# Kernel optimization log

Hardware: AMD Instinct MI355X
Metric: run time of the kernel (lower is better)

## Reference

```python
import jax, jax.numpy as jnp
import numpy as np


def swiglu(g, u):
    return jax.nn.silu(g) * u


def setup_inputs() -> dict:
    key = jax.random.key(0)
    ks = jax.random.split(key, 10)
    D, H, E, HS = 2048, 512, 32, 1024
    B, S = 1, 2048
    s = 0.02
    return {
        "x": jax.random.normal(ks[0], (B, S, D), jnp.float32),
        "gate_w": jax.random.normal(ks[1], (E, D), jnp.float32) * s,
        "expert_bias": jnp.zeros((E,), jnp.float32),
        "wg": jax.random.normal(ks[2], (E, D, H), jnp.float32) * s,
        "wu": jax.random.normal(ks[3], (E, D, H), jnp.float32) * s,
        "wd": jax.random.normal(ks[4], (E, H, D), jnp.float32) * s,
        "sg": jax.random.normal(ks[5], (D, HS), jnp.float32) * s,
        "su": jax.random.normal(ks[6], (D, HS), jnp.float32) * s,
        "sd": jax.random.normal(ks[7], (HS, D), jnp.float32) * s,
        "coef_w": jax.random.normal(ks[8], (2, D), jnp.float32) * s,
        "coef_b": jnp.zeros((2,), jnp.float32),
        "top_k": 4,
    }


def reference(x, gate_w, expert_bias, wg, wu, wd, sg, su, sd, coef_w, coef_b, top_k):
    # --- sigmoid router with bias-adjusted top-k selection ---
    logits = jnp.einsum("bsd,ed->bse", x, gate_w)            # [B,S,E]
    routing = jax.nn.sigmoid(logits.astype(jnp.float32))
    biased = routing + expert_bias[None, None, :]
    _, inds = jax.lax.top_k(biased, top_k)                    # [B,S,k]
    scores = jnp.take_along_axis(routing, inds, axis=-1)      # gather UNbiased weights
    scores = scores / (jnp.sum(scores, axis=-1, keepdims=True) + 1e-20)  # norm_topk_prob
    scores = scores.astype(x.dtype)

    # --- SwitchGLU experts: dense per-expert SwiGLU, then gather top-k outputs ---
    h = jnp.einsum("bsd,edh->bseh", x, wg)                    # [B,S,E,H]
    u = jnp.einsum("bsd,edh->bseh", x, wu)
    y_all = jnp.einsum("bseh,ehd->bsed", swiglu(h, u), wd)    # [B,S,E,D]
    expert_out = jnp.take_along_axis(
        y_all, inds[..., None], axis=2)                        # [B,S,k,D]
    y_experts = jnp.sum(expert_out * scores[..., None], axis=-2)  # [B,S,D]

    # --- shared expert + learned 2-way mixing coefficient ---
    shared = swiglu(x @ sg, x @ su) @ sd                      # [B,S,D]
    coef = jax.nn.softmax(jnp.einsum("bsd,cd->bsc", x, coef_w) + coef_b, axis=-1)
    return y_experts * coef[..., :1] + shared * coef[..., 1:]
```

## Files before the change

kernel.cpp:

```cpp
#include <hip/hip_runtime.h>
#include <hip/hip_bf16.h>
#include <stdint.h>

#define S_TOK   2048
#define DMODEL  2048
#define HEXP    512
#define NEXP    32
#define HSH     1024
#define NPAIR   (S_TOK * 4)
#define NT128   96
#define NT64    160

#define M128_NT  0
#define M128_TE  1
#define M128_TP0 (1 + NT128)
#define M128_TM  (1 + 2 * NT128)
#define M64_NT   (1 + 3 * NT128)
#define M64_TE   (M64_NT + 1)
#define M64_TP0  (M64_NT + 1 + NT64)
#define M64_TM   (M64_NT + 1 + 2 * NT64)
#define META_SIZE (M64_NT + 1 + 3 * NT64)

typedef short  s16x8 __attribute__((ext_vector_type(8)));
typedef __bf16 b16x8 __attribute__((ext_vector_type(8)));
typedef float  f32x4 __attribute__((ext_vector_type(4)));

__device__ __forceinline__ f32x4 mfma16x16x32(s16x8 a, s16x8 b, f32x4 c) {
    return __builtin_amdgcn_mfma_f32_16x16x32_bf16(
        __builtin_bit_cast(b16x8, a), __builtin_bit_cast(b16x8, b), c, 0, 0, 0);
}

__device__ __forceinline__ unsigned short f2bf(float f) {
    union { float f; unsigned int u; } v; v.f = f;
    unsigned int u = v.u;
    return (unsigned short)((u + 0x7FFFu + ((u >> 16) & 1u)) >> 16);
}

__device__ __forceinline__ float bf2f(unsigned short b) {
    union { unsigned int u; float f; } v; v.u = ((unsigned int)b) << 16;
    return v.f;
}

__device__ __forceinline__ void gload16(const unsigned short* g, unsigned short* l) {
    __builtin_amdgcn_global_load_lds(
        (const __attribute__((address_space(1))) void*)(uintptr_t)g,
        (__attribute__((address_space(3))) void*)(uintptr_t)l, 16, 0, 0);
}

__device__ __forceinline__ int src_col8(int lane) {
    return 8 * ((lane & 3) ^ ((lane >> 3) & 3));
}
__device__ __forceinline__ int frag_ko(int fr, int fq) {
    return 8 * (fq ^ ((fr >> 1) & 3));
}

__device__ __forceinline__ void tconv_tile(const float* __restrict__ s,
                                           unsigned short* __restrict__ d,
                                           const int K, const int N,
                                           const int k0, const int n0,
                                           unsigned short* pool)
{
    auto T = (unsigned short (*)[84])pool;
    const int tid = threadIdx.x;
    const int n4 = (tid & 15) * 4;
    const int kr = tid >> 4;
#pragma unroll
    for (int i = 0; i < 4; ++i) {
        const int k = kr + i * 16;
        const float4 v = *reinterpret_cast<const float4*>(s + (size_t)(k0 + k) * N + n0 + n4);
        T[n4 + 0][k] = f2bf(v.x);
        T[n4 + 1][k] = f2bf(v.y);
        T[n4 + 2][k] = f2bf(v.z);
        T[n4 + 3][k] = f2bf(v.w);
    }
    __syncthreads();
    const int nw = tid >> 2;
    const int kc = (tid & 3) * 16;
    unsigned short* o = d + (size_t)(n0 + nw) * K + k0 + kc;
#pragma unroll
    for (int j = 0; j < 4; ++j)
        *reinterpret_cast<uint2*>(o + j * 4) =
            *reinterpret_cast<const uint2*>(&T[nw][kc + j * 4]);
}

__global__ __launch_bounds__(256)
void router_kernel(const float* __restrict__ x, const float* __restrict__ gate_w,
                   const float* __restrict__ expert_bias,
                   const float* __restrict__ coef_w, const float* __restrict__ coef_b,
                   int* __restrict__ inds, float* __restrict__ scores,
                   float* __restrict__ coefo)
{
    const int t = blockIdx.x;
    const int tid = threadIdx.x;
    const int lane = tid & 63;
    const int wave = tid >> 6;
    const float* xr = x + (size_t)t * DMODEL;

    float xv[32];
#pragma unroll
    for (int j = 0; j < 32; ++j) xv[j] = xr[lane + 64 * j];

    __shared__ float s_logits[NEXP];
    __shared__ float s_coef[2];

    for (int i = 0; i < 8; ++i) {
        const int e = wave * 8 + i;
        const float* wr = gate_w + (size_t)e * DMODEL;
        float p = 0.f;
#pragma unroll
        for (int j = 0; j < 32; ++j) p += xv[j] * wr[lane + 64 * j];
#pragma unroll
        for (int o = 32; o > 0; o >>= 1) p += __shfl_xor(p, o);
        if (lane == 0) s_logits[e] = p;
    }
    if (wave == 0) {
        for (int c = 0; c < 2; ++c) {
            const float* wr = coef_w + (size_t)c * DMODEL;
            float p = 0.f;
#pragma unroll
            for (int j = 0; j < 32; ++j) p += xv[j] * wr[lane + 64 * j];
#pragma unroll
            for (int o = 32; o > 0; o >>= 1) p += __shfl_xor(p, o);
            if (lane == 0) s_coef[c] = p;
        }
    }
    __syncthreads();
    if (tid == 0) {
        float routing[NEXP], biased[NEXP];
        for (int e = 0; e < NEXP; ++e) {
            const float r = 1.f / (1.f + expf(-s_logits[e]));
            routing[e] = r;
            biased[e] = r + expert_bias[e];
        }
        int sel[4]; float sc[4]; float ssum = 0.f;
        for (int k = 0; k < 4; ++k) {
            int best = 0; float bv = -1e30f;
            for (int e = 0; e < NEXP; ++e)
                if (biased[e] > bv) { bv = biased[e]; best = e; }
            sel[k] = best; sc[k] = routing[best]; ssum += sc[k];
            biased[best] = -1e30f;
        }
        const float inv = 1.f / (ssum + 1e-20f);
        for (int k = 0; k < 4; ++k) {
            inds[t * 4 + k] = sel[k];
            scores[t * 4 + k] = sc[k] * inv;
        }
        const float l0 = s_coef[0] + coef_b[0];
        const float l1 = s_coef[1] + coef_b[1];
        const float m = fmaxf(l0, l1);
        const float e0 = expf(l0 - m), e1 = expf(l1 - m);
        coefo[t * 2 + 0] = e0 / (e0 + e1);
        coefo[t * 2 + 1] = e1 / (e0 + e1);
    }
}

__global__ __launch_bounds__(256)
void xcast_kernel(const float* __restrict__ x, unsigned short* __restrict__ xb)
{
    const int i = (blockIdx.x * 256 + threadIdx.x) * 4;
    const float4 v = *reinterpret_cast<const float4*>(x + i);
    ushort4 o;
    o.x = f2bf(v.x); o.y = f2bf(v.y); o.z = f2bf(v.z); o.w = f2bf(v.w);
    *reinterpret_cast<ushort4*>(xb + i) = o;
}

__global__ __launch_bounds__(256)
void tconv_all_kernel(const float* __restrict__ wg, const float* __restrict__ wu,
                      const float* __restrict__ sg, const float* __restrict__ su,
                      const float* __restrict__ sd,
                      unsigned short* __restrict__ W1, unsigned short* __restrict__ W2,
                      unsigned short* __restrict__ sgb, unsigned short* __restrict__ sub_,
                      unsigned short* __restrict__ sdb)
{
    __shared__ unsigned short pool[64 * 84];
    const int bid = blockIdx.x;
    if (bid < 8192) {
        const int e = bid >> 8, t = bid & 255;
        tconv_tile(wg + (size_t)e * DMODEL * HEXP, W1 + (size_t)e * HEXP * DMODEL,
                   DMODEL, HEXP, ((t >> 3) & 31) * 64, (t & 7) * 64, pool);
    } else if (bid < 16384) {
        const int e = (bid - 8192) >> 8, t = bid & 255;
        tconv_tile(wu + (size_t)e * DMODEL * HEXP, W2 + (size_t)e * HEXP * DMODEL,
                   DMODEL, HEXP, ((t >> 3) & 31) * 64, (t & 7) * 64, pool);
    } else if (bid < 16896) {
        const int t = bid - 16384;
        tconv_tile(sg, sgb, DMODEL, HSH, (t >> 4) * 64, (t & 15) * 64, pool);
    } else if (bid < 17408) {
        const int t = bid - 16896;
        tconv_tile(su, sub_, DMODEL, HSH, (t >> 4) * 64, (t & 15) * 64, pool);
    } else {
        const int t = bid - 17408;
        tconv_tile(sd, sdb, HSH, DMODEL, (t >> 5) * 64, (t & 31) * 64, pool);
    }
}

__global__ __launch_bounds__(256)
void tconv_wd_kernel(const float* __restrict__ wd, unsigned short* __restrict__ wdb)
{
    __shared__ unsigned short pool[64 * 84];
    const int e = blockIdx.x >> 8, t = blockIdx.x & 255;
    tconv_tile(wd + (size_t)e * HEXP * DMODEL, wdb + (size_t)e * DMODEL * HEXP,
               HEXP, DMODEL, (t >> 5) * 64, (t & 31) * 64, pool);
}

__global__ __launch_bounds__(1024)
void group_kernel(const int* __restrict__ inds, const float* __restrict__ scores,
                  int* __restrict__ meta, int* __restrict__ pair_token,
                  float* __restrict__ pair_score, int* __restrict__ tok_pos)
{
    __shared__ int cnt[NEXP];
    __shared__ int off_s[NEXP];
    __shared__ int cur[NEXP];
    const int tid = threadIdx.x;
    if (tid < NEXP) cnt[tid] = 0;
    __syncthreads();
    for (int i = tid; i < NPAIR; i += 1024) atomicAdd(&cnt[inds[i]], 1);
    __syncthreads();
    if (tid == 0) {
        int run = 0, nt1 = 0, nt2 = 0;
        for (int e = 0; e < NEXP; ++e) {
            off_s[e] = run;
            const int c = cnt[e];
            for (int m0 = 0; m0 < c; m0 += 128) {
                meta[M128_TE + nt1] = e;
                meta[M128_TP0 + nt1] = run + m0;
                meta[M128_TM + nt1] = (c - m0 < 128) ? (c - m0) : 128;
                ++nt1;
            }
            for (int m0 = 0; m0 < c; m0 += 64) {
                meta[M64_TE + nt2] = e;
                meta[M64_TP0 + nt2] = run + m0;
                meta[M64_TM + nt2] = (c - m0 < 64) ? (c - m0) : 64;
                ++nt2;
            }
            run += c;
        }
        meta[M128_NT] = nt1;
        meta[M64_NT] = nt2;
    }
    __syncthreads();
    if (tid < NEXP) cur[tid] = off_s[tid];
    __syncthreads();
    for (int i = tid; i < NPAIR; i += 1024) {
        const int e = inds[i];
        const int pos = atomicAdd(&cur[e], 1);
        pair_token[pos] = i >> 2;
        pair_score[pos] = scores[i];
        tok_pos[i] = pos;
    }
}

__global__ __launch_bounds__(256, 4)
void gufused_kernel(const unsigned short* __restrict__ xb,
                    const unsigned short* __restrict__ W1,
                    const unsigned short* __restrict__ W2,
                    unsigned short* __restrict__ act,
                    const int* __restrict__ meta, const int* __restrict__ pair_token,
                    const unsigned short* __restrict__ sgb,
                    const unsigned short* __restrict__ sub_,
                    unsigned short* __restrict__ shact)
{
    __shared__ unsigned short pool[16384];
    const int bid = blockIdx.x;
    const int tid = threadIdx.x;
    const int lane = tid & 63;
    const int wave = tid >> 6;
    const int fr = lane & 15, fq = lane >> 4;
    const int ko = frag_ko(fr, fq);
    const int sub = lane >> 2;
    const int col8 = src_col8(lane);
    const f32x4 zero4 = {0.f, 0.f, 0.f, 0.f};

    if (bid < 8 * NT128) {
        constexpr int NT = DMODEL / 32;
        constexpr int NB = HEXP;
        auto Al  = (unsigned short (*)[128][32])(pool);
        auto Bgl = (unsigned short (*)[64][32])(pool + 8192);
        auto Bul = (unsigned short (*)[64][32])(pool + 12288);

        const int tt = bid >> 3;
        if (tt >= meta[M128_NT]) return;
        const int e = meta[M128_TE + tt];
        const int p0 = meta[M128_TP0 + tt];
        const int mval = meta[M128_TM + tt];
        const size_t eoff = (size_t)e * NB * DMODEL;
        const unsigned short* Bg = W1 + eoff;
        const unsigned short* Bu = W2 + eoff;
        const int n0 = (bid & 7) * 64;

        const int arow0 = wave * 32 + sub;
        int q0 = p0 + arow0; if (q0 > NPAIR - 1) q0 = NPAIR - 1;
        int q1 = p0 + arow0 + 16; if (q1 > NPAIR - 1) q1 = NPAIR - 1;
        const unsigned short* asrc0 = xb + (size_t)pair_token[q0] * DMODEL + col8;
        const unsigned short* asrc1 = xb + (size_t)pair_token[q1] * DMODEL + col8;
        const int brow = wave * 16 + sub;
        const unsigned short* gsrc = Bg + (size_t)(n0 + brow) * DMODEL + col8;
        const unsigned short* usrc = Bu + (size_t)(n0 + brow) * DMODEL + col8;

        auto stage = [&](int buf, int k0) {
            gload16(asrc0 + k0, &Al[buf][wave * 32][0]);
            gload16(asrc1 + k0, &Al[buf][wave * 32 + 16][0]);
            gload16(gsrc + k0, &Bgl[buf][wave * 16][0]);
            gload16(usrc + k0, &Bul[buf][wave * 16][0]);
        };

        const int wm = wave >> 1, wn = wave & 1;
        f32x4 hacc[4][2], uacc[4][2];
#pragma unroll
        for (int m = 0; m < 4; ++m)
#pragma unroll
            for (int n = 0; n < 2; ++n) { hacc[m][n] = zero4; uacc[m][n] = zero4; }

        auto compute = [&](int buf) {
            s16x8 af[4], bg[2], bu[2];
#pragma unroll
            for (int m = 0; m < 4; ++m)
                af[m] = *reinterpret_cast<const s16x8*>(&Al[buf][wm * 64 + m * 16 + fr][ko]);
#pragma unroll
            for (int n = 0; n < 2; ++n) {
                bg[n] = *reinterpret_cast<const s16x8*>(&Bgl[buf][wn * 32 + n * 16 + fr][ko]);
                bu[n] = *reinterpret_cast<const s16x8*>(&Bul[buf][wn * 32 + n * 16 + fr][ko]);
            }
#pragma unroll
            for (int m = 0; m < 4; ++m)
#pragma unroll
                for (int n = 0; n < 2; ++n) {
                    hacc[m][n] = mfma16x16x32(af[m], bg[n], hacc[m][n]);
                    uacc[m][n] = mfma16x16x32(af[m], bu[n], uacc[m][n]);
                }
        };

        stage(0, 0);
        __syncthreads();
#pragma unroll 1
        for (int t = 0; t < NT; ++t) {
            const int cur = t & 1;
            if (t + 1 < NT) stage(cur ^ 1, (t + 1) * 32);
            compute(cur);
            __syncthreads();
        }

#pragma unroll
        for (int m = 0; m < 4; ++m)
#pragma unroll
            for (int n = 0; n < 2; ++n) {
                const int col = n0 + wn * 32 + n * 16 + fr;
#pragma unroll
                for (int r = 0; r < 4; ++r) {
                    const int rt = wm * 64 + m * 16 + fq * 4 + r;
                    if (rt < mval) {
                        const float hv = hacc[m][n][r];
                        const float a = hv / (1.f + __expf(-hv)) * uacc[m][n][r];
                        act[(size_t)(p0 + rt) * NB + col] = f2bf(a);
                    }
                }
            }
    } else {
        constexpr int NT = DMODEL / 32;
        constexpr int NB = HSH;
        auto Al  = (unsigned short (*)[64][32])(pool);
        auto Bgl = (unsigned short (*)[64][32])(pool + 4096);
        auto Bul = (unsigned short (*)[64][32])(pool + 8192);

        const int idx = bid - 8 * NT128;
        const int p0 = (idx >> 4) * 64;
        const int n0 = (idx & 15) * 64;

        const int arow = wave * 16 + sub;
        const unsigned short* asrc = xb + (size_t)(p0 + arow) * DMODEL + col8;
        const unsigned short* gsrc = sgb + (size_t)(n0 + arow) * DMODEL + col8;
        const unsigned short* usrc = sub_ + (size_t)(n0 + arow) * DMODEL + col8;

        auto stage = [&](int buf, int k0) {
            gload16(asrc + k0, &Al[buf][wave * 16][0]);
            gload16(gsrc + k0, &Bgl[buf][wave * 16][0]);
            gload16(usrc + k0, &Bul[buf][wave * 16][0]);
        };

        const int wm = wave >> 1, wn = wave & 1;
        f32x4 hacc[2][2], uacc[2][2];
#pragma unroll
        for (int m = 0; m < 2; ++m)
#pragma unroll
            for (int n = 0; n < 2; ++n) { hacc[m][n] = zero4; uacc[m][n] = zero4; }

        auto compute = [&](int buf) {
            s16x8 af[2], bg[2], bu[2];
#pragma unroll
            for (int m = 0; m < 2; ++m)
                af[m] = *reinterpret_cast<const s16x8*>(&Al[buf][wm * 32 + m * 16 + fr][ko]);
#pragma unroll
            for (int n = 0; n < 2; ++n) {
                bg[n] = *reinterpret_cast<const s16x8*>(&Bgl[buf][wn * 32 + n * 16 + fr][ko]);
                bu[n] = *reinterpret_cast<const s16x8*>(&Bul[buf][wn * 32 + n * 16 + fr][ko]);
            }
#pragma unroll
            for (int m = 0; m < 2; ++m)
#pragma unroll
                for (int n = 0; n < 2; ++n) {
                    hacc[m][n] = mfma16x16x32(af[m], bg[n], hacc[m][n]);
                    uacc[m][n] = mfma16x16x32(af[m], bu[n], uacc[m][n]);
                }
        };

        stage(0, 0);
        __syncthreads();
#pragma unroll 1
        for (int t = 0; t < NT; ++t) {
            const int cur = t & 1;
            if (t + 1 < NT) stage(cur ^ 1, (t + 1) * 32);
            compute(cur);
            __syncthreads();
        }

#pragma unroll
        for (int m = 0; m < 2; ++m)
#pragma unroll
            for (int n = 0; n < 2; ++n) {
                const int col = n0 + wn * 32 + n * 16 + fr;
#pragma unroll
                for (int r = 0; r < 4; ++r) {
                    const int rt = wm * 32 + m * 16 + fq * 4 + r;
                    const float hv = hacc[m][n][r];
                    const float a = hv / (1.f + __expf(-hv)) * uacc[m][n][r];
                    shact[(size_t)(p0 + rt) * NB + col] = f2bf(a);
                }
            }
    }
}

__global__ __launch_bounds__(256, 4)
void downfused_kernel(const unsigned short* __restrict__ act,
                      const unsigned short* __restrict__ shact,
                      const unsigned short* __restrict__ wdb,
                      const unsigned short* __restrict__ sdb,
                      unsigned short* __restrict__ ypair,
                      float* __restrict__ sdown,
                      const int* __restrict__ meta,
                      const float* __restrict__ pair_score)
{
    __shared__ unsigned short Al[2][64][32];
    __shared__ unsigned short Bl[2][64][32];
    const int bid = blockIdx.x;
    const int tid = threadIdx.x;
    const int lane = tid & 63;
    const int wave = tid >> 6;
    const int fr = lane & 15, fq = lane >> 4;
    const int ko = frag_ko(fr, fq);
    const int sub = lane >> 2;
    const int col8 = src_col8(lane);
    const int wm = wave >> 1, wn = wave & 1;
    const f32x4 zero4 = {0.f, 0.f, 0.f, 0.f};

    const bool EXPERT = bid < 32 * NT64;
    int p0, mval, n0, KA;
    const unsigned short *Asrc, *Bd;
    if (EXPERT) {
        const int tt = bid >> 5;
        if (tt >= meta[M64_NT]) return;
        const int e = meta[M64_TE + tt];
        p0 = meta[M64_TP0 + tt];
        mval = meta[M64_TM + tt];
        n0 = (bid & 31) * 64;
        KA = HEXP;
        Asrc = act;
        Bd = wdb + (size_t)e * DMODEL * HEXP;
    } else {
        const int idx = bid - 32 * NT64;
        p0 = (idx >> 5) * 64;
        mval = 64;
        n0 = (idx & 31) * 64;
        KA = HSH;
        Asrc = shact;
        Bd = sdb;
    }
    const int NT = KA / 32;

    const int arow = wave * 16 + sub;
    int ar = p0 + arow;
    if (EXPERT && ar > NPAIR - 1) ar = NPAIR - 1;
    const unsigned short* asrc = Asrc + (size_t)ar * KA + col8;
    const unsigned short* bsrc = Bd + (size_t)(n0 + arow) * KA + col8;

    auto stage = [&](int buf, int k0) {
        gload16(asrc + k0, &Al[buf][wave * 16][0]);
        gload16(bsrc + k0, &Bl[buf][wave * 16][0]);
    };

    f32x4 acc[2][2];
#pragma unroll
    for (int m = 0; m < 2; ++m)
#pragma unroll
        for (int n = 0; n < 2; ++n) acc[m][n] = zero4;

    auto compute = [&](int buf) {
        s16x8 af[2], bf[2];
#pragma unroll
        for (int m = 0; m < 2; ++m)
            af[m] = *reinterpret_cast<const s16x8*>(&Al[buf][wm * 32 + m * 16 + fr][ko]);
#pragma unroll
        for (int n = 0; n < 2; ++n)
            bf[n] = *reinterpret_cast<const s16x8*>(&Bl[buf][wn * 32 + n * 16 + fr][ko]);
#pragma unroll
        for (int m = 0; m < 2; ++m)
#pragma unroll
            for (int n = 0; n < 2; ++n)
                acc[m][n] = mfma16x16x32(af[m], bf[n], acc[m][n]);
    };

    stage(0, 0);
    __syncthreads();
#pragma unroll 1
    for (int t = 0; t < NT; ++t) {
        const int cur = t & 1;
        if (t + 1 < NT) stage(cur ^ 1, (t + 1) * 32);
        compute(cur);
        __syncthreads();
    }

#pragma unroll
    for (int m = 0; m < 2; ++m)
#pragma unroll
        for (int n = 0; n < 2; ++n) {
            const int col = n0 + wn * 32 + n * 16 + fr;
#pragma unroll
            for (int r = 0; r < 4; ++r) {
                const int rt = wm * 32 + m * 16 + fq * 4 + r;
                if (rt < mval) {
                    if (EXPERT) {
                        const int p = p0 + rt;
                        ypair[(size_t)p * DMODEL + col] = f2bf(acc[m][n][r] * pair_score[p]);
                    } else {
                        sdown[(size_t)(p0 + rt) * DMODEL + col] = acc[m][n][r];
                    }
                }
            }
        }
}

__global__ __launch_bounds__(256)
void final_kernel(const unsigned short* __restrict__ ypair,
                  const float* __restrict__ sdown,
                  const float* __restrict__ coef, const int* __restrict__ tok_pos,
                  float* __restrict__ out)
{
    const int row = blockIdx.x;
    const int col = threadIdx.x * 8;
    float acc[8] = {0.f, 0.f, 0.f, 0.f, 0.f, 0.f, 0.f, 0.f};
#pragma unroll
    for (int k = 0; k < 4; ++k) {
        const int pos = tok_pos[row * 4 + k];
        const uint4 v = *reinterpret_cast<const uint4*>(ypair + (size_t)pos * DMODEL + col);
        const unsigned short* u = reinterpret_cast<const unsigned short*>(&v);
#pragma unroll
        for (int j = 0; j < 8; ++j) acc[j] += bf2f(u[j]);
    }
    const float c0 = coef[row * 2 + 0];
    const float c1 = coef[row * 2 + 1];
    const float* sd = sdown + (size_t)row * DMODEL + col;
    const float4 s0 = *reinterpret_cast<const float4*>(sd);
    const float4 s1 = *reinterpret_cast<const float4*>(sd + 4);
    float4 o0, o1;
    o0.x = acc[0] * c0 + s0.x * c1; o0.y = acc[1] * c0 + s0.y * c1;
    o0.z = acc[2] * c0 + s0.z * c1; o0.w = acc[3] * c0 + s0.w * c1;
    o1.x = acc[4] * c0 + s1.x * c1; o1.y = acc[5] * c0 + s1.y * c1;
    o1.z = acc[6] * c0 + s1.z * c1; o1.w = acc[7] * c0 + s1.w * c1;
    float* op = out + (size_t)row * DMODEL + col;
    *reinterpret_cast<float4*>(op) = o0;
    *reinterpret_cast<float4*>(op + 4) = o1;
}

extern "C" void kernel_launch(void* const* d_in, const int* in_sizes, int n_in,
                              void* d_out, int out_size, void* d_ws, size_t ws_size,
                              hipStream_t stream)
{
    const float* x           = (const float*)d_in[0];
    const float* gate_w      = (const float*)d_in[1];
    const float* expert_bias = (const float*)d_in[2];
    const float* wg          = (const float*)d_in[3];
    const float* wu          = (const float*)d_in[4];
    const float* wd          = (const float*)d_in[5];
    const float* sg          = (const float*)d_in[6];
    const float* su          = (const float*)d_in[7];
    const float* sd          = (const float*)d_in[8];
    const float* coef_w      = (const float*)d_in[9];
    const float* coef_b      = (const float*)d_in[10];
    float* out = (float*)d_out;

    char* ws = (char*)d_ws;
    size_t off = 0;
    auto take = [&](size_t bytes) {
        char* p = ws + off;
        off = (off + bytes + 255) & ~(size_t)255;
        return p;
    };
    int*   inds     = (int*)  take((size_t)S_TOK * 4 * sizeof(int));
    float* scores   = (float*)take((size_t)S_TOK * 4 * sizeof(float));
    float* coefp    = (float*)take((size_t)S_TOK * 2 * sizeof(float));
    int*   meta     = (int*)  take((size_t)META_SIZE * sizeof(int));
    int*   pair_tok = (int*)  take((size_t)NPAIR * sizeof(int));
    float* pair_sc  = (float*)take((size_t)NPAIR * sizeof(float));
    int*   tok_pos  = (int*)  take((size_t)NPAIR * sizeof(int));
    unsigned short* xb    = (unsigned short*)take((size_t)S_TOK * DMODEL * 2);
    unsigned short* act   = (unsigned short*)take((size_t)NPAIR * HEXP * 2);
    unsigned short* shact = (unsigned short*)take((size_t)S_TOK * HSH * 2);
    unsigned short* ypair = (unsigned short*)take((size_t)NPAIR * DMODEL * 2);
    float*          sdown = (float*)take((size_t)S_TOK * DMODEL * 4);
    unsigned short* sgb   = (unsigned short*)take((size_t)HSH * DMODEL * 2);
    unsigned short* sub_  = (unsigned short*)take((size_t)HSH * DMODEL * 2);
    unsigned short* sdb   = (unsigned short*)take((size_t)DMODEL * HSH * 2);
    unsigned short* W1    = (unsigned short*)take((size_t)NEXP * DMODEL * HEXP * 2);
    unsigned short* W2    = (unsigned short*)take((size_t)NEXP * DMODEL * HEXP * 2);
    (void)ws_size; (void)in_sizes; (void)n_in; (void)out_size;

    router_kernel<<<S_TOK, 256, 0, stream>>>(x, gate_w, expert_bias, coef_w, coef_b,
                                             inds, scores, coefp);
    xcast_kernel<<<(S_TOK * DMODEL / 4) / 256, 256, 0, stream>>>(x, xb);
    group_kernel<<<1, 1024, 0, stream>>>(inds, scores, meta, pair_tok, pair_sc, tok_pos);

    tconv_all_kernel<<<17920, 256, 0, stream>>>(wg, wu, sg, su, sd,
                                                W1, W2, sgb, sub_, sdb);

    gufused_kernel<<<8 * NT128 + 512, 256, 0, stream>>>(
        xb, W1, W2, act, meta, pair_tok, sgb, sub_, shact);

    tconv_wd_kernel<<<NEXP * 256, 256, 0, stream>>>(wd, W1);

    downfused_kernel<<<32 * NT64 + 1024, 256, 0, stream>>>(
        act, shact, W1, sdb, ypair, sdown, meta, pair_sc);

    final_kernel<<<S_TOK, 256, 0, stream>>>(ypair, sdown, coefp, tok_pos, out);
}
```

Baseline: 360.5 us.

## Use 128x128 GEMM tiles for gate/up and down, split SwiGLU into separate pass

Gate and up projections now run as separate 128x128-tile GEMMs that write bf16 h and u to scratch buffers. A new elementwise kernel applies SwiGLU to produce the activations. The down projection moves from 64x64 to 128x128 tiles on the 128-row expert grouping, and the 64-row metadata is removed. Larger tiles raise arithmetic intensity and reuse of each loaded tile, at the cost of an extra round trip through memory for h/u, an extra kernel launch, more padding waste on partial expert tiles, and higher register pressure (launch bounds reduced to 3).

```diff
diff --git a/kernel.cpp b/kernel.cpp
--- a/kernel.cpp
+++ b/kernel.cpp
@@ -9,17 +9,12 @@
 #define HSH     1024
 #define NPAIR   (S_TOK * 4)
 #define NT128   96
-#define NT64    160
 
 #define M128_NT  0
 #define M128_TE  1
 #define M128_TP0 (1 + NT128)
 #define M128_TM  (1 + 2 * NT128)
-#define M64_NT   (1 + 3 * NT128)
-#define M64_TE   (M64_NT + 1)
-#define M64_TP0  (M64_NT + 1 + NT64)
-#define M64_TM   (M64_NT + 1 + 2 * NT64)
-#define META_SIZE (M64_NT + 1 + 3 * NT64)
+#define META_SIZE (1 + 3 * NT128)
 
 typedef short  s16x8 __attribute__((ext_vector_type(8)));
 typedef __bf16 b16x8 __attribute__((ext_vector_type(8)));
@@ -217,7 +212,7 @@
     for (int i = tid; i < NPAIR; i += 1024) atomicAdd(&cnt[inds[i]], 1);
     __syncthreads();
     if (tid == 0) {
-        int run = 0, nt1 = 0, nt2 = 0;
+        int run = 0, nt1 = 0;
         for (int e = 0; e < NEXP; ++e) {
             off_s[e] = run;
             const int c = cnt[e];
@@ -227,16 +222,9 @@
                 meta[M128_TM + nt1] = (c - m0 < 128) ? (c - m0) : 128;
                 ++nt1;
             }
-            for (int m0 = 0; m0 < c; m0 += 64) {
-                meta[M64_TE + nt2] = e;
-                meta[M64_TP0 + nt2] = run + m0;
-                meta[M64_TM + nt2] = (c - m0 < 64) ? (c - m0) : 64;
-                ++nt2;
-            }
             run += c;
         }
         meta[M128_NT] = nt1;
-        meta[M64_NT] = nt2;
     }
     __syncthreads();
     if (tid < NEXP) cur[tid] = off_s[tid];
@@ -250,197 +238,20 @@
     }
 }
 
-__global__ __launch_bounds__(256, 4)
-void gufused_kernel(const unsigned short* __restrict__ xb,
-                    const unsigned short* __restrict__ W1,
-                    const unsigned short* __restrict__ W2,
-                    unsigned short* __restrict__ act,
-                    const int* __restrict__ meta, const int* __restrict__ pair_token,
-                    const unsigned short* __restrict__ sgb,
-                    const unsigned short* __restrict__ sub_,
-                    unsigned short* __restrict__ shact)
-{
-    __shared__ unsigned short pool[16384];
-    const int bid = blockIdx.x;
-    const int tid = threadIdx.x;
-    const int lane = tid & 63;
-    const int wave = tid >> 6;
-    const int fr = lane & 15, fq = lane >> 4;
-    const int ko = frag_ko(fr, fq);
-    const int sub = lane >> 2;
-    const int col8 = src_col8(lane);
-    const f32x4 zero4 = {0.f, 0.f, 0.f, 0.f};
-
-    if (bid < 8 * NT128) {
-        constexpr int NT = DMODEL / 32;
-        constexpr int NB = HEXP;
-        auto Al  = (unsigned short (*)[128][32])(pool);
-        auto Bgl = (unsigned short (*)[64][32])(pool + 8192);
-        auto Bul = (unsigned short (*)[64][32])(pool + 12288);
-
-        const int tt = bid >> 3;
-        if (tt >= meta[M128_NT]) return;
-        const int e = meta[M128_TE + tt];
-        const int p0 = meta[M128_TP0 + tt];
-        const int mval = meta[M128_TM + tt];
-        const size_t eoff = (size_t)e * NB * DMODEL;
-        const unsigned short* Bg = W1 + eoff;
-        const unsigned short* Bu = W2 + eoff;
-        const int n0 = (bid & 7) * 64;
-
-        const int arow0 = wave * 32 + sub;
-        int q0 = p0 + arow0; if (q0 > NPAIR - 1) q0 = NPAIR - 1;
-        int q1 = p0 + arow0 + 16; if (q1 > NPAIR - 1) q1 = NPAIR - 1;
-        const unsigned short* asrc0 = xb + (size_t)pair_token[q0] * DMODEL + col8;
-        const unsigned short* asrc1 = xb + (size_t)pair_token[q1] * DMODEL + col8;
-        const int brow = wave * 16 + sub;
-        const unsigned short* gsrc = Bg + (size_t)(n0 + brow) * DMODEL + col8;
-        const unsigned short* usrc = Bu + (size_t)(n0 + brow) * DMODEL + col8;
-
-        auto stage = [&](int buf, int k0) {
-            gload16(asrc0 + k0, &Al[buf][wave * 32][0]);
-            gload16(asrc1 + k0, &Al[buf][wave * 32 + 16][0]);
-            gload16(gsrc + k0, &Bgl[buf][wave * 16][0]);
-            gload16(usrc + k0, &Bul[buf][wave * 16][0]);
-        };
-
-        const int wm = wave >> 1, wn = wave & 1;
-        f32x4 hacc[4][2], uacc[4][2];
-#pragma unroll
-        for (int m = 0; m < 4; ++m)
-#pragma unroll
-            for (int n = 0; n < 2; ++n) { hacc[m][n] = zero4; uacc[m][n] = zero4; }
-
-        auto compute = [&](int buf) {
-            s16x8 af[4], bg[2], bu[2];
-#pragma unroll
-            for (int m = 0; m < 4; ++m)
-                af[m] = *reinterpret_cast<const s16x8*>(&Al[buf][wm * 64 + m * 16 + fr][ko]);
-#pragma unroll
-            for (int n = 0; n < 2; ++n) {
-                bg[n] = *reinterpret_cast<const s16x8*>(&Bgl[buf][wn * 32 + n * 16 + fr][ko]);
-                bu[n] = *reinterpret_cast<const s16x8*>(&Bul[buf][wn * 32 + n * 16 + fr][ko]);
-            }
-#pragma unroll
-            for (int m = 0; m < 4; ++m)
-#pragma unroll
-                for (int n = 0; n < 2; ++n) {
-                    hacc[m][n] = mfma16x16x32(af[m], bg[n], hacc[m][n]);
-                    uacc[m][n] = mfma16x16x32(af[m], bu[n], uacc[m][n]);
-                }
-        };
-
-        stage(0, 0);
-        __syncthreads();
-#pragma unroll 1
-        for (int t = 0; t < NT; ++t) {
-            const int cur = t & 1;
-            if (t + 1 < NT) stage(cur ^ 1, (t + 1) * 32);
-            compute(cur);
-            __syncthreads();
-        }
-
-#pragma unroll
-        for (int m = 0; m < 4; ++m)
-#pragma unroll
-            for (int n = 0; n < 2; ++n) {
-                const int col = n0 + wn * 32 + n * 16 + fr;
-#pragma unroll
-                for (int r = 0; r < 4; ++r) {
-                    const int rt = wm * 64 + m * 16 + fq * 4 + r;
-                    if (rt < mval) {
-                        const float hv = hacc[m][n][r];
-                        const float a = hv / (1.f + __expf(-hv)) * uacc[m][n][r];
-                        act[(size_t)(p0 + rt) * NB + col] = f2bf(a);
-                    }
-                }
-            }
-    } else {
-        constexpr int NT = DMODEL / 32;
-        constexpr int NB = HSH;
-        auto Al  = (unsigned short (*)[64][32])(pool);
-        auto Bgl = (unsigned short (*)[64][32])(pool + 4096);
-        auto Bul = (unsigned short (*)[64][32])(pool + 8192);
-
-        const int idx = bid - 8 * NT128;
-        const int p0 = (idx >> 4) * 64;
-        const int n0 = (idx & 15) * 64;
-
-        const int arow = wave * 16 + sub;
-        const unsigned short* asrc = xb + (size_t)(p0 + arow) * DMODEL + col8;
-        const unsigned short* gsrc = sgb + (size_t)(n0 + arow) * DMODEL + col8;
-        const unsigned short* usrc = sub_ + (size_t)(n0 + arow) * DMODEL + col8;
-
-        auto stage = [&](int buf, int k0) {
-            gload16(asrc + k0, &Al[buf][wave * 16][0]);
-            gload16(gsrc + k0, &Bgl[buf][wave * 16][0]);
-            gload16(usrc + k0, &Bul[buf][wave * 16][0]);
-        };
-
-        const int wm = wave >> 1, wn = wave & 1;
-        f32x4 hacc[2][2], uacc[2][2];
-#pragma unroll
-        for (int m = 0; m < 2; ++m)
-#pragma unroll
-            for (int n = 0; n < 2; ++n) { hacc[m][n] = zero4; uacc[m][n] = zero4; }
-
-        auto compute = [&](int buf) {
-            s16x8 af[2], bg[2], bu[2];
-#pragma unroll
-            for (int m = 0; m < 2; ++m)
-                af[m] = *reinterpret_cast<const s16x8*>(&Al[buf][wm * 32 + m * 16 + fr][ko]);
-#pragma unroll
-            for (int n = 0; n < 2; ++n) {
-                bg[n] = *reinterpret_cast<const s16x8*>(&Bgl[buf][wn * 32 + n * 16 + fr][ko]);
-                bu[n] = *reinterpret_cast<const s16x8*>(&Bul[buf][wn * 32 + n * 16 + fr][ko]);
-            }
-#pragma unroll
-            for (int m = 0; m < 2; ++m)
-#pragma unroll
-                for (int n = 0; n < 2; ++n) {
-                    hacc[m][n] = mfma16x16x32(af[m], bg[n], hacc[m][n]);
-                    uacc[m][n] = mfma16x16x32(af[m], bu[n], uacc[m][n]);
-                }
-        };
-
-        stage(0, 0);
-        __syncthreads();
-#pragma unroll 1
-        for (int t = 0; t < NT; ++t) {
-            const int cur = t & 1;
-            if (t + 1 < NT) stage(cur ^ 1, (t + 1) * 32);
-            compute(cur);
-            __syncthreads();
-        }
-
-#pragma unroll
-        for (int m = 0; m < 2; ++m)
-#pragma unroll
-            for (int n = 0; n < 2; ++n) {
-                const int col = n0 + wn * 32 + n * 16 + fr;
-#pragma unroll
-                for (int r = 0; r < 4; ++r) {
-                    const int rt = wm * 32 + m * 16 + fq * 4 + r;
-                    const float hv = hacc[m][n][r];
-                    const float a = hv / (1.f + __expf(-hv)) * uacc[m][n][r];
-                    shact[(size_t)(p0 + rt) * NB + col] = f2bf(a);
-                }
-            }
-    }
-}
-
-__global__ __launch_bounds__(256, 4)
-void downfused_kernel(const unsigned short* __restrict__ act,
-                      const unsigned short* __restrict__ shact,
-                      const unsigned short* __restrict__ wdb,
-                      const unsigned short* __restrict__ sdb,
-                      unsigned short* __restrict__ ypair,
-                      float* __restrict__ sdown,
-                      const int* __restrict__ meta,
-                      const float* __restrict__ pair_score)
-{
-    __shared__ unsigned short Al[2][64][32];
-    __shared__ unsigned short Bl[2][64][32];
+__global__ __launch_bounds__(256, 3)
+void gu128_kernel(const unsigned short* __restrict__ xb,
+                  const unsigned short* __restrict__ W1,
+                  const unsigned short* __restrict__ W2,
+                  const int* __restrict__ meta, const int* __restrict__ pair_token,
+                  const unsigned short* __restrict__ sgb,
+                  const unsigned short* __restrict__ sub_,
+                  unsigned short* __restrict__ hexp, unsigned short* __restrict__ uexp,
+                  unsigned short* __restrict__ shh, unsigned short* __restrict__ shu)
+{
+    constexpr int NT = DMODEL / 32;
+    __shared__ unsigned short Al[2][128][32];
+    __shared__ unsigned short Bl[2][128][32];
+
     const int bid = blockIdx.x;
     const int tid = threadIdx.x;
     const int lane = tid & 63;
@@ -452,59 +263,71 @@
     const int wm = wave >> 1, wn = wave & 1;
     const f32x4 zero4 = {0.f, 0.f, 0.f, 0.f};
 
-    const bool EXPERT = bid < 32 * NT64;
-    int p0, mval, n0, KA;
-    const unsigned short *Asrc, *Bd;
+    const bool EXPERT = bid < 8 * NT128;
+    int p0, mval, n0, NB;
+    const unsigned short* B;
+    unsigned short* obuf;
+    int tok0, tok1;
+    const int arow0 = wave * 32 + sub;
     if (EXPERT) {
-        const int tt = bid >> 5;
-        if (tt >= meta[M64_NT]) return;
-        const int e = meta[M64_TE + tt];
-        p0 = meta[M64_TP0 + tt];
-        mval = meta[M64_TM + tt];
-        n0 = (bid & 31) * 64;
-        KA = HEXP;
-        Asrc = act;
-        Bd = wdb + (size_t)e * DMODEL * HEXP;
+        const int tt = bid >> 3;
+        if (tt >= meta[M128_NT]) return;
+        const int e = meta[M128_TE + tt];
+        p0 = meta[M128_TP0 + tt];
+        mval = meta[M128_TM + tt];
+        const int r = bid & 7;
+        const int mat = r >> 2;
+        n0 = (r & 3) * 128;
+        NB = HEXP;
+        B = (mat ? W2 : W1) + (size_t)e * HEXP * DMODEL;
+        obuf = mat ? uexp : hexp;
+        int q0 = p0 + arow0;      if (q0 > NPAIR - 1) q0 = NPAIR - 1;
+        int q1 = p0 + arow0 + 16; if (q1 > NPAIR - 1) q1 = NPAIR - 1;
+        tok0 = pair_token[q0];
+        tok1 = pair_token[q1];
     } else {
-        const int idx = bid - 32 * NT64;
-        p0 = (idx >> 5) * 64;
-        mval = 64;
-        n0 = (idx & 31) * 64;
-        KA = HSH;
-        Asrc = shact;
-        Bd = sdb;
-    }
-    const int NT = KA / 32;
-
-    const int arow = wave * 16 + sub;
-    int ar = p0 + arow;
-    if (EXPERT && ar > NPAIR - 1) ar = NPAIR - 1;
-    const unsigned short* asrc = Asrc + (size_t)ar * KA + col8;
-    const unsigned short* bsrc = Bd + (size_t)(n0 + arow) * KA + col8;
+        const int idx = bid - 8 * NT128;
+        const int mat = idx & 1;
+        n0 = ((idx >> 1) & 7) * 128;
+        p0 = (idx >> 4) * 128;
+        mval = 128;
+        NB = HSH;
+        B = mat ? sub_ : sgb;
+        obuf = mat ? shu : shh;
+        tok0 = p0 + arow0;
+        tok1 = p0 + arow0 + 16;
+    }
+
+    const unsigned short* asrc0 = xb + (size_t)tok0 * DMODEL + col8;
+    const unsigned short* asrc1 = xb + (size_t)tok1 * DMODEL + col8;
+    const unsigned short* bsrc0 = B + (size_t)(n0 + arow0) * DMODEL + col8;
+    const unsigned short* bsrc1 = B + (size_t)(n0 + arow0 + 16) * DMODEL + col8;
 
     auto stage = [&](int buf, int k0) {
-        gload16(asrc + k0, &Al[buf][wave * 16][0]);
-        gload16(bsrc + k0, &Bl[buf][wave * 16][0]);
+        gload16(asrc0 + k0, &Al[buf][wave * 32][0]);
+        gload16(asrc1 + k0, &Al[buf][wave * 32 + 16][0]);
+        gload16(bsrc0 + k0, &Bl[buf][wave * 32][0]);
+        gload16(bsrc1 + k0, &Bl[buf][wave * 32 + 16][0]);
     };
 
-    f32x4 acc[2][2];
-#pragma unroll
-    for (int m = 0; m < 2; ++m)
-#pragma unroll
-        for (int n = 0; n < 2; ++n) acc[m][n] = zero4;
+    f32x4 acc[4][4];
+#pragma unroll
+    for (int m = 0; m < 4; ++m)
+#pragma unroll
+        for (int n = 0; n < 4; ++n) acc[m][n] = zero4;
 
     auto compute = [&](int buf) {
-        s16x8 af[2], bf[2];
-#pragma unroll
-        for (int m = 0; m < 2; ++m)
-            af[m] = *reinterpret_cast<const s16x8*>(&Al[buf][wm * 32 + m * 16 + fr][ko]);
-#pragma unroll
-        for (int n = 0; n < 2; ++n)
-            bf[n] = *reinterpret_cast<const s16x8*>(&Bl[buf][wn * 32 + n * 16 + fr][ko]);
-#pragma unroll
-        for (int m = 0; m < 2; ++m)
-#pragma unroll
-            for (int n = 0; n < 2; ++n)
+        s16x8 af[4], bf[4];
+#pragma unroll
+        for (int m = 0; m < 4; ++m)
+            af[m] = *reinterpret_cast<const s16x8*>(&Al[buf][wm * 64 + m * 16 + fr][ko]);
+#pragma unroll
+        for (int n = 0; n < 4; ++n)
+            bf[n] = *reinterpret_cast<const s16x8*>(&Bl[buf][wn * 64 + n * 16 + fr][ko]);
+#pragma unroll
+        for (int m = 0; m < 4; ++m)
+#pragma unroll
+            for (int n = 0; n < 4; ++n)
                 acc[m][n] = mfma16x16x32(af[m], bf[n], acc[m][n]);
     };
 
@@ -519,13 +342,149 @@
     }
 
 #pragma unroll
-    for (int m = 0; m < 2; ++m)
-#pragma unroll
-        for (int n = 0; n < 2; ++n) {
-            const int col = n0 + wn * 32 + n * 16 + fr;
+    for (int m = 0; m < 4; ++m)
+#pragma unroll
+        for (int n = 0; n < 4; ++n) {
+            const int col = n0 + wn * 64 + n * 16 + fr;
 #pragma unroll
             for (int r = 0; r < 4; ++r) {
-                const int rt = wm * 32 + m * 16 + fq * 4 + r;
+                const int rt = wm * 64 + m * 16 + fq * 4 + r;
+                if (rt < mval)
+                    obuf[(size_t)(p0 + rt) * NB + col] = f2bf(acc[m][n][r]);
+            }
+        }
+}
+
+__global__ __launch_bounds__(256)
+void swiglu_kernel(const unsigned short* __restrict__ hexp,
+                   const unsigned short* __restrict__ uexp,
+                   unsigned short* __restrict__ act,
+                   const unsigned short* __restrict__ shh,
+                   const unsigned short* __restrict__ shu,
+                   unsigned short* __restrict__ shact)
+{
+    constexpr size_t NE = (size_t)NPAIR * HEXP;
+    const size_t i = ((size_t)blockIdx.x * 256 + threadIdx.x) * 8;
+    const unsigned short *hp, *up;
+    unsigned short* ap;
+    size_t j;
+    if (i < NE) { hp = hexp; up = uexp; ap = act; j = i; }
+    else        { hp = shh;  up = shu;  ap = shact; j = i - NE; }
+    const uint4 hv = *reinterpret_cast<const uint4*>(hp + j);
+    const uint4 uv = *reinterpret_cast<const uint4*>(up + j);
+    const unsigned short* hu = reinterpret_cast<const unsigned short*>(&hv);
+    const unsigned short* uu = reinterpret_cast<const unsigned short*>(&uv);
+    ushort4 o[2];
+    unsigned short* ou = reinterpret_cast<unsigned short*>(o);
+#pragma unroll
+    for (int k = 0; k < 8; ++k) {
+        const float h = bf2f(hu[k]);
+        const float u = bf2f(uu[k]);
+        ou[k] = f2bf(h / (1.f + __expf(-h)) * u);
+    }
+    *reinterpret_cast<uint4*>(ap + j) = *reinterpret_cast<const uint4*>(o);
+}
+
+__global__ __launch_bounds__(256, 3)
+void down128_kernel(const unsigned short* __restrict__ act,
+                    const unsigned short* __restrict__ shact,
+                    const unsigned short* __restrict__ wdb,
+                    const unsigned short* __restrict__ sdb,
+                    unsigned short* __restrict__ ypair,
+                    float* __restrict__ sdown,
+                    const int* __restrict__ meta,
+                    const float* __restrict__ pair_score)
+{
+    __shared__ unsigned short Al[2][128][32];
+    __shared__ unsigned short Bl[2][128][32];
+
+    const int bid = blockIdx.x;
+    const int tid = threadIdx.x;
+    const int lane = tid & 63;
+    const int wave = tid >> 6;
+    const int fr = lane & 15, fq = lane >> 4;
+    const int ko = frag_ko(fr, fq);
+    const int sub = lane >> 2;
+    const int col8 = src_col8(lane);
+    const int wm = wave >> 1, wn = wave & 1;
+    const f32x4 zero4 = {0.f, 0.f, 0.f, 0.f};
+
+    const bool EXPERT = bid < 16 * NT128;
+    int p0, mval, n0, KA;
+    const unsigned short *Asrc, *B;
+    if (EXPERT) {
+        const int tt = bid >> 4;
+        if (tt >= meta[M128_NT]) return;
+        const int e = meta[M128_TE + tt];
+        p0 = meta[M128_TP0 + tt];
+        mval = meta[M128_TM + tt];
+        n0 = (bid & 15) * 128;
+        KA = HEXP;
+        Asrc = act;
+        B = wdb + (size_t)e * DMODEL * HEXP;
+    } else {
+        const int idx = bid - 16 * NT128;
+        p0 = (idx >> 4) * 128;
+        mval = 128;
+        n0 = (idx & 15) * 128;
+        KA = HSH;
+        Asrc = shact;
+        B = sdb;
+    }
+    const int NT = KA / 32;
+
+    const int arow0 = wave * 32 + sub;
+    const unsigned short* asrc0 = Asrc + (size_t)(p0 + arow0) * KA + col8;
+    const unsigned short* asrc1 = Asrc + (size_t)(p0 + arow0 + 16) * KA + col8;
+    const unsigned short* bsrc0 = B + (size_t)(n0 + arow0) * KA + col8;
+    const unsigned short* bsrc1 = B + (size_t)(n0 + arow0 + 16) * KA + col8;
+
+    auto stage = [&](int buf, int k0) {
+        gload16(asrc0 + k0, &Al[buf][wave * 32][0]);
+        gload16(asrc1 + k0, &Al[buf][wave * 32 + 16][0]);
+        gload16(bsrc0 + k0, &Bl[buf][wave * 32][0]);
+        gload16(bsrc1 + k0, &Bl[buf][wave * 32 + 16][0]);
+    };
+
+    f32x4 acc[4][4];
+#pragma unroll
+    for (int m = 0; m < 4; ++m)
+#pragma unroll
+        for (int n = 0; n < 4; ++n) acc[m][n] = zero4;
+
+    auto compute = [&](int buf) {
+        s16x8 af[4], bf[4];
+#pragma unroll
+        for (int m = 0; m < 4; ++m)
+            af[m] = *reinterpret_cast<const s16x8*>(&Al[buf][wm * 64 + m * 16 + fr][ko]);
+#pragma unroll
+        for (int n = 0; n < 4; ++n)
+            bf[n] = *reinterpret_cast<const s16x8*>(&Bl[buf][wn * 64 + n * 16 + fr][ko]);
+#pragma unroll
+        for (int m = 0; m < 4; ++m)
+#pragma unroll
+            for (int n = 0; n < 4; ++n)
+                acc[m][n] = mfma16x16x32(af[m], bf[n], acc[m][n]);
+    };
+
+    stage(0, 0);
+    __syncthreads();
+#pragma unroll 1
+    for (int t = 0; t < NT; ++t) {
+        const int cur = t & 1;
+        if (t + 1 < NT) stage(cur ^ 1, (t + 1) * 32);
+        compute(cur);
+        __syncthreads();
+    }
+
+#pragma unroll
+    for (int m = 0; m < 4; ++m)
+#pragma unroll
+        for (int n = 0; n < 4; ++n) {
+            const int col = n0 + wn * 64 + n * 16 + fr;
+#pragma unroll
+            for (int r = 0; r < 4; ++r) {
+                const int rt = wm * 64 + m * 16 + fq * 4 + r;
                 if (rt < mval) {
                     if (EXPERT) {
                         const int p = p0 + rt;
@@ -603,7 +562,11 @@
     int*   tok_pos  = (int*)  take((size_t)NPAIR * sizeof(int));
     unsigned short* xb    = (unsigned short*)take((size_t)S_TOK * DMODEL * 2);
     unsigned short* act   = (unsigned short*)take((size_t)NPAIR * HEXP * 2);
+    unsigned short* hexp  = (unsigned short*)take((size_t)NPAIR * HEXP * 2);
+    unsigned short* uexp  = (unsigned short*)take((size_t)NPAIR * HEXP * 2);
     unsigned short* shact = (unsigned short*)take((size_t)S_TOK * HSH * 2);
+    unsigned short* shh   = (unsigned short*)take((size_t)S_TOK * HSH * 2);
+    unsigned short* shu   = (unsigned short*)take((size_t)S_TOK * HSH * 2);
     unsigned short* ypair = (unsigned short*)take((size_t)NPAIR * DMODEL * 2);
     float*          sdown = (float*)take((size_t)S_TOK * DMODEL * 4);
     unsigned short* sgb   = (unsigned short*)take((size_t)HSH * DMODEL * 2);
@@ -621,12 +584,14 @@
     tconv_all_kernel<<<17920, 256, 0, stream>>>(wg, wu, sg, su, sd,
                                                 W1, W2, sgb, sub_, sdb);
 
-    gufused_kernel<<<8 * NT128 + 512, 256, 0, stream>>>(
-        xb, W1, W2, act, meta, pair_tok, sgb, sub_, shact);
+    gu128_kernel<<<8 * NT128 + 256, 256, 0, stream>>>(
+        xb, W1, W2, meta, pair_tok, sgb, sub_, hexp, uexp, shh, shu);
+
+    swiglu_kernel<<<3072, 256, 0, stream>>>(hexp, uexp, act, shh, shu, shact);
 
     tconv_wd_kernel<<<NEXP * 256, 256, 0, stream>>>(wd, W1);
 
-    downfused_kernel<<<32 * NT64 + 1024, 256, 0, stream>>>(
+    down128_kernel<<<16 * NT128 + 256, 256, 0, stream>>>(
         act, shact, W1, sdb, ypair, sdown, meta, pair_sc);
 
     final_kernel<<<S_TOK, 256, 0, stream>>>(ypair, sdown, coefp, tok_pos, out);
```

Measured after the change: 348.8 us. -3.2%, faster.
